# Kernel tuning notes

Hardware: AMD Instinct MI355X
Metric: run time of the kernel (lower is better)

## Reference

```python
import jax, jax.numpy as jnp
import numpy as np

N = 100_000   # nodes
E = 3_200_000 # edges (avg degree 32)
F_NODE = 64
F_EDGE = 16
HID = 64
NEG_SLOPE = 0.2


def _gat_conv(x, src, dst, edge_attr, W, a_src, a_dst, We, a_e, bias, n):
    """PyG GATConv (heads=1, edge_dim, add_self_loops=True fill='mean', eval mode)."""
    # --- add self loops; loop edge_attr = mean of incoming edge_attr per node ---
    deg = jax.ops.segment_sum(jnp.ones((src.shape[0],), x.dtype), dst, num_segments=n)
    loop_attr = jax.ops.segment_sum(edge_attr, dst, num_segments=n)
    loop_attr = jnp.where(deg[:, None] > 0, loop_attr / jnp.maximum(deg, 1.0)[:, None], 0.0)
    loop = jnp.arange(n, dtype=src.dtype)
    src2 = jnp.concatenate([src, loop])
    dst2 = jnp.concatenate([dst, loop])
    ea = jnp.concatenate([edge_attr, loop_attr], axis=0)

    # --- node / edge projections and per-node attention terms ---
    h = x @ W                                   # [N, HID]
    alpha_src = h @ a_src                       # [N]
    alpha_dst = h @ a_dst                       # [N]
    e = ea @ We                                 # [E+N, HID]
    alpha_e = e @ a_e                           # [E+N]

    # --- per-edge logits + segment softmax over destination neighborhoods ---
    logits = jax.nn.leaky_relu(alpha_src[src2] + alpha_dst[dst2] + alpha_e, NEG_SLOPE)
    seg_max = jax.ops.segment_max(logits, dst2, num_segments=n)  # every node has self loop
    ex = jnp.exp(logits - seg_max[dst2])
    denom = jax.ops.segment_sum(ex, dst2, num_segments=n)
    w = ex / denom[dst2]                        # [E+N]

    # --- weighted scatter-aggregate of messages ---
    out = jax.ops.segment_sum(h[src2] * w[:, None], dst2, num_segments=n)
    return out + bias


def setup_inputs() -> dict:
    key = jax.random.key(0)
    ks = jax.random.split(key, 16)
    s = 0.1  # keep logits tame
    return {
        "x": jax.random.normal(ks[0], (N, F_NODE), jnp.float32),
        "edge_index": jax.random.randint(ks[1], (2, E), 0, N, jnp.int32),
        "edge_attr": jax.random.normal(ks[2], (E, F_EDGE), jnp.float32),
        "W1": jax.random.normal(ks[3], (F_NODE, HID), jnp.float32) * s,
        "att_src1": jax.random.normal(ks[4], (HID,), jnp.float32) * s,
        "att_dst1": jax.random.normal(ks[5], (HID,), jnp.float32) * s,
        "We1": jax.random.normal(ks[6], (F_EDGE, HID), jnp.float32) * s,
        "att_edge1": jax.random.normal(ks[7], (HID,), jnp.float32) * s,
        "b1": jnp.zeros((HID,), jnp.float32),
        "W2": jax.random.normal(ks[8], (HID, HID), jnp.float32) * s,
        "att_src2": jax.random.normal(ks[9], (HID,), jnp.float32) * s,
        "att_dst2": jax.random.normal(ks[10], (HID,), jnp.float32) * s,
        "We2": jax.random.normal(ks[11], (F_EDGE, HID), jnp.float32) * s,
        "att_edge2": jax.random.normal(ks[12], (HID,), jnp.float32) * s,
        "b2": jnp.zeros((HID,), jnp.float32),
        "fc_w": jax.random.normal(ks[13], (HID, 1), jnp.float32) * s,
        "fc_b": jnp.zeros((1,), jnp.float32),
    }


def reference(x, edge_index, edge_attr, W1, att_src1, att_dst1, We1, att_edge1, b1,
              W2, att_src2, att_dst2, We2, att_edge2, b2, fc_w, fc_b):
    src, dst = edge_index[0], edge_index[1]
    n = x.shape[0]
    h = jax.nn.elu(_gat_conv(x, src, dst, edge_attr, W1, att_src1, att_dst1, We1, att_edge1, b1, n))
    h = jax.nn.elu(_gat_conv(h, src, dst, edge_attr, W2, att_src2, att_dst2, We2, att_edge2, b2, n))
    return h @ fc_w + fc_b  # [N, 1] logits
```

## Files before the change

kernel.cpp:

```cpp
#include <hip/hip_runtime.h>
#include <hip/hip_bf16.h>
#include <hip/hip_fp16.h>
#include <math.h>
#include <stdint.h>

constexpr int HIDDIM = 64;
constexpr int FEDGE  = 16;
constexpr int BN     = 512;
constexpr int CAP    = 17000;
constexpr int TILE   = 4096;
constexpr int NTA    = 512;
constexpr int EPT    = TILE / NTA;

__global__ void compute_c_kernel(const float* __restrict__ We1, const float* __restrict__ ae1,
                                 const float* __restrict__ We2, const float* __restrict__ ae2,
                                 float* __restrict__ c) {
  int t = threadIdx.x;
  if (t < FEDGE) {
    float s = 0.f;
    for (int j = 0; j < HIDDIM; ++j) s += We1[t * HIDDIM + j] * ae1[j];
    c[t] = s;
  } else if (t < 2 * FEDGE) {
    int k = t - FEDGE;
    float s = 0.f;
    for (int j = 0; j < HIDDIM; ++j) s += We2[k * HIDDIM + j] * ae2[j];
    c[FEDGE + k] = s;
  }
}

__device__ __forceinline__ int pack_ae(float a1, float a2) {
  unsigned lo = __half_as_ushort(__float2half_rn(a1));
  unsigned hi = __half_as_ushort(__float2half_rn(a2));
  return (int)((hi << 16) | lo);
}
template <int SEL>
__device__ __forceinline__ float unpack_ae(int pk) {
  unsigned u = (SEL == 0) ? ((unsigned)pk & 0xFFFFu) : ((unsigned)pk >> 16);
  return __half2float(__ushort_as_half((unsigned short)u));
}

__global__ __launch_bounds__(NTA) void passA_kernel(
    const int* __restrict__ src, const int* __restrict__ dst,
    const float* __restrict__ attr, const float* __restrict__ c,
    int* __restrict__ bucketCursor, int2* __restrict__ P, int E, int nbuck) {
  __shared__ int st_ae[TILE];
  __shared__ int s_key[TILE];
  __shared__ int s_ae[TILE];
  __shared__ unsigned char s_b[TILE];
  __shared__ int cnt[256];
  __shared__ int lbase[512];
  __shared__ int gbase[256];
  __shared__ int wsum[8];
  __shared__ float cs[32];
  int t = threadIdx.x;
  if (t < 32) cs[t] = c[t];
  if (t < nbuck) cnt[t] = 0;
  __syncthreads();
  int e0 = blockIdx.x * TILE;
  int tileCnt = min(TILE, E - e0);

  int d_reg[EPT];
#pragma unroll
  for (int k = 0; k < EPT; ++k) {
    int e = e0 + k * NTA + t;
    d_reg[k] = (e < E) ? dst[e] : -1;
  }
#pragma unroll
  for (int k = 0; k < EPT; ++k) {
    if (d_reg[k] >= 0) atomicAdd(&cnt[d_reg[k] >> 9], 1);
  }
  __syncthreads();

  int lane = t & 63, w = t >> 6;
  int n = (t < nbuck) ? cnt[t] : 0;
  int ret = 0;
  if (n > 0) ret = atomicAdd(&bucketCursor[t], n);
  int incl = n;
#pragma unroll
  for (int d = 1; d < 64; d <<= 1) {
    int tv = __shfl_up(incl, d, 64);
    if (lane >= d) incl += tv;
  }
  if (lane == 63) wsum[w] = incl;
  __syncthreads();
  {
    int woff = 0;
#pragma unroll
    for (int w2 = 0; w2 < 8; ++w2) woff += (w2 < w) ? wsum[w2] : 0;
    lbase[t] = incl - n + woff;
    if (t < nbuck) { gbase[t] = ret; cnt[t] = 0; }
  }

  {
    int q   = t & 3;
    int grp = t >> 2;
    const float4* attr4 = (const float4*)attr;
#pragma unroll
    for (int pass = 0; pass < TILE / 128; ++pass) {
      int el = pass * 128 + grp;
      int e = e0 + el;
      float4 v = make_float4(0.f, 0.f, 0.f, 0.f);
      if (e < E) v = attr4[(size_t)e * 4 + q];
      float a1 = v.x * cs[4*q]    + v.y * cs[4*q+1]    + v.z * cs[4*q+2]    + v.w * cs[4*q+3];
      float a2 = v.x * cs[16+4*q] + v.y * cs[16+4*q+1] + v.z * cs[16+4*q+2] + v.w * cs[16+4*q+3];
      a1 += __shfl_xor(a1, 1, 64); a1 += __shfl_xor(a1, 2, 64);
      a2 += __shfl_xor(a2, 1, 64); a2 += __shfl_xor(a2, 2, 64);
      if (q == 0) st_ae[el] = pack_ae(a1, a2);
    }
  }
  __syncthreads();

#pragma unroll
  for (int k = 0; k < EPT; ++k) {
    int d = d_reg[k];
    if (d < 0) continue;
    int el = k * NTA + t;
    int e = e0 + el;
    int b = d >> 9;
    int sE = src[e];
    int r = atomicAdd(&cnt[b], 1);
    int idx = lbase[b] + r;
    s_key[idx] = sE | ((d & 511) << 20);
    s_ae[idx]  = st_ae[el];
    s_b[idx]   = (unsigned char)b;
  }
  __syncthreads();

  for (int i = t; i < tileCnt; i += NTA) {
    int b = s_b[i];
    int rank = i - lbase[b];
    int pos = gbase[b] + rank;
    if (pos < CAP) P[(size_t)b * CAP + pos] = make_int2(s_key[i], s_ae[i]);
  }
}

__global__ void scan_buckets_kernel(const int* __restrict__ bucketCursor,
                                    int* __restrict__ bucketBase,
                                    int* __restrict__ offsets, int nbuck, int N, int E) {
  __shared__ int s[512];
  int t = threadIdx.x;
  int v = (t < nbuck) ? min(bucketCursor[t], CAP) : 0;
  s[t] = v;
  __syncthreads();
  for (int d = 1; d < 512; d <<= 1) {
    int tv = (t >= d) ? s[t - d] : 0;
    __syncthreads();
    s[t] += tv;
    __syncthreads();
  }
  if (t < nbuck) bucketBase[t] = s[t] - v;
  if (t == 0) offsets[N] = E;
}

__global__ __launch_bounds__(512) void passB_kernel(
    const int2* __restrict__ P, const int* __restrict__ bucketCursor,
    const int* __restrict__ bucketBase, int* __restrict__ offsets,
    int2* __restrict__ EDGS, int N) {
  int b = blockIdx.x;
  int t = threadIdx.x;
  int nodeBase = b * BN;
  int cnt = min(bucketCursor[b], CAP);
  int gbase = bucketBase[b];
  __shared__ int hist[BN];
  __shared__ int cur[BN];
  __shared__ int wsum[8];
  hist[t] = 0;
  __syncthreads();
  const int2* Pb = P + (size_t)b * CAP;
  for (int i = t; i < cnt; i += 512) {
    int dl = (Pb[i].x >> 20) & 511;
    atomicAdd(&hist[dl], 1);
  }
  __syncthreads();
  int deg = hist[t];
  int lane = t & 63, w = t >> 6;
  int incl = deg;
#pragma unroll
  for (int d = 1; d < 64; d <<= 1) {
    int tv = __shfl_up(incl, d, 64);
    if (lane >= d) incl += tv;
  }
  if (lane == 63) wsum[w] = incl;
  __syncthreads();
  int woff = 0;
#pragma unroll
  for (int w2 = 0; w2 < 8; ++w2) woff += (w2 < w) ? wsum[w2] : 0;
  int excl = incl - deg + woff;
  int nodeId = nodeBase + t;
  if (nodeId < N) offsets[nodeId] = gbase + excl;
  cur[t] = gbase + excl;
  __syncthreads();
  for (int i = t; i < cnt; i += 512) {
    int2 r = Pb[i];
    int dl = (r.x >> 20) & 511;
    int pos = atomicAdd(&cur[dl], 1);
    EDGS[pos] = r;
  }
}

template <bool IN16>
__global__ __launch_bounds__(256) void gemm_alpha_kernel(
    const void* __restrict__ Xv, const float* __restrict__ W,
    const float* __restrict__ a_src, const float* __restrict__ a_dst,
    __half2* __restrict__ H, float* __restrict__ alpha_s, float* __restrict__ alpha_d, int n) {
  __shared__ float Ws[HIDDIM * HIDDIM];
  __shared__ float as_s[HIDDIM], ad_s[HIDDIM];
  for (int i = threadIdx.x; i < HIDDIM * HIDDIM; i += blockDim.x) Ws[i] = W[i];
  if (threadIdx.x < HIDDIM) {
    as_s[threadIdx.x] = a_src[threadIdx.x];
    ad_s[threadIdx.x] = a_dst[threadIdx.x];
  }
  __syncthreads();
  int lane = threadIdx.x & 63;
  int wid  = threadIdx.x >> 6;
  int wavesTotal = (blockDim.x >> 6) * gridDim.x;
  for (int row = blockIdx.x * (blockDim.x >> 6) + wid; row < n; row += wavesTotal) {
    float xv;
    if (IN16) xv = __half2float(((const __half*)Xv)[(size_t)row * HIDDIM + lane]);
    else      xv = ((const float*)Xv)[(size_t)row * HIDDIM + lane];
    float acc = 0.f;
#pragma unroll
    for (int k = 0; k < HIDDIM; ++k) {
      float xk = __shfl(xv, k, 64);
      acc = fmaf(xk, Ws[k * HIDDIM + lane], acc);
    }
    float accN = __shfl_xor(acc, 1, 64);
    if (!(lane & 1)) {
      H[(size_t)row * 32 + (lane >> 1)] = __floats2half2_rn(acc, accN);
    }
    float s1 = acc * as_s[lane];
    float s2 = acc * ad_s[lane];
#pragma unroll
    for (int d = 32; d > 0; d >>= 1) {
      s1 += __shfl_xor(s1, d, 64);
      s2 += __shfl_xor(s2, d, 64);
    }
    if (lane == 0) {
      alpha_s[row] = s1;
      alpha_d[row] = s2;
    }
  }
}

__device__ __forceinline__ float leaky(float x) { return (x < 0.f) ? 0.2f * x : x; }
__device__ __forceinline__ float elu(float x) { return (x > 0.f) ? x : (__expf(x) - 1.f); }

template <bool FINAL, int SEL>
__global__ __launch_bounds__(256) void aggregate_kernel(
    const __half2* __restrict__ H, const float* __restrict__ alpha_s, const float* __restrict__ alpha_d,
    const int2* __restrict__ EDGS, const int* __restrict__ offsets,
    const float* __restrict__ bias, const float* __restrict__ fc_w, const float* __restrict__ fc_b,
    void* __restrict__ out, int n) {
  int lane = threadIdx.x & 63;
  int wid  = threadIdx.x >> 6;
  int node = blockIdx.x * (blockDim.x >> 6) + wid;
  if (node >= n) return;
  int off = offsets[node];
  int deg = offsets[node + 1] - off;
  float ad  = alpha_d[node];
  float asn = alpha_s[node];

  if (deg <= 64) {
    int2 ed = make_int2(0, 0);
    if (lane < deg) ed = EDGS[off + lane];
    int   s_l  = ed.x & 0xFFFFF;
    float ae_l = unpack_ae<SEL>(ed.y);
    float as_g = (lane < deg) ? alpha_s[s_l] : 0.f;
    float lg_l = (lane < deg) ? leaky(as_g + ad + ae_l) : -INFINITY;
    float aesum = (lane < deg) ? ae_l : 0.f;
    float lmax = lg_l;
#pragma unroll
    for (int d = 32; d > 0; d >>= 1) {
      lmax = fmaxf(lmax, __shfl_xor(lmax, d, 64));
      aesum += __shfl_xor(aesum, d, 64);
    }
    float self_ae = (deg > 0) ? aesum / (float)deg : 0.f;
    float slg = leaky(asn + ad + self_ae);
    float m = fmaxf(lmax, slg);

    float ex_l = (lane < deg) ? __expf(lg_l - m) : 0.f;
    float dsum = ex_l;
#pragma unroll
    for (int d = 32; d > 0; d >>= 1) dsum += __shfl_xor(dsum, d, 64);
    float exs = __expf(slg - m);
    float denom = dsum + exs;

    int half = lane >> 5;
    int c32  = lane & 31;

    float selfw = (half == 0) ? exs : 0.f;
    float2 hv = __half22float2(H[(size_t)node * 32 + c32]);
    float2 acc2;
    acc2.x = selfw * hv.x;
    acc2.y = selfw * hv.y;

    int jj = 0;
    for (; jj + 16 <= deg; jj += 16) {
      int   si[8]; float ei[8];
#pragma unroll
      for (int k = 0; k < 8; ++k) {
        si[k] = __shfl(s_l, jj + 2 * k + half, 64);
        ei[k] = __shfl(ex_l, jj + 2 * k + half, 64);
      }
      float2 hh[8];
#pragma unroll
      for (int k = 0; k < 8; ++k) hh[k] = __half22float2(H[(size_t)si[k] * 32 + c32]);
#pragma unroll
      for (int k = 0; k < 8; ++k) {
        acc2.x = fmaf(ei[k], hh[k].x, acc2.x);
        acc2.y = fmaf(ei[k], hh[k].y, acc2.y);
      }
    }
    for (; jj + 8 <= deg; jj += 8) {
      int j0 = jj + half, j1 = jj + 2 + half, j2 = jj + 4 + half, j3 = jj + 6 + half;
      int   sa = __shfl(s_l, j0, 64),  sb = __shfl(s_l, j1, 64);
      int   sc = __shfl(s_l, j2, 64),  sd = __shfl(s_l, j3, 64);
      float ea = __shfl(ex_l, j0, 64), eb = __shfl(ex_l, j1, 64);
      float ec = __shfl(ex_l, j2, 64), ef = __shfl(ex_l, j3, 64);
      float2 ha = __half22float2(H[(size_t)sa * 32 + c32]);
      float2 hb = __half22float2(H[(size_t)sb * 32 + c32]);
      float2 hc = __half22float2(H[(size_t)sc * 32 + c32]);
      float2 hd = __half22float2(H[(size_t)sd * 32 + c32]);
      acc2.x = fmaf(ea, ha.x, acc2.x); acc2.y = fmaf(ea, ha.y, acc2.y);
      acc2.x = fmaf(eb, hb.x, acc2.x); acc2.y = fmaf(eb, hb.y, acc2.y);
      acc2.x = fmaf(ec, hc.x, acc2.x); acc2.y = fmaf(ec, hc.y, acc2.y);
      acc2.x = fmaf(ef, hd.x, acc2.x); acc2.y = fmaf(ef, hd.y, acc2.y);
    }
    for (; jj < deg; jj += 2) {
      int j = jj + half;
      int   sj = __shfl(s_l, j, 64);
      float ej = __shfl(ex_l, j, 64);
      float2 hj = __half22float2(H[(size_t)sj * 32 + c32]);
      acc2.x = fmaf(ej, hj.x, acc2.x);
      acc2.y = fmaf(ej, hj.y, acc2.y);
    }
    acc2.x += __shfl_xor(acc2.x, 32, 64);
    acc2.y += __shfl_xor(acc2.y, 32, 64);

    const float2* bi2 = (const float2*)bias;
    float2 bv = bi2[c32];
    float rx = elu(acc2.x / denom + bv.x);
    float ry = elu(acc2.y / denom + bv.y);
    if (!FINAL) {
      if (half == 0) {
        ((__half2*)out)[(size_t)node * 32 + c32] = __floats2half2_rn(rx, ry);
      }
    } else {
      const float2* fw2 = (const float2*)fc_w;
      float2 fv = fw2[c32];
      float s1 = rx * fv.x + ry * fv.y;
#pragma unroll
      for (int d = 16; d > 0; d >>= 1) s1 += __shfl_xor(s1, d, 64);
      if (lane == 0) ((float*)out)[node] = s1 + fc_b[0];
    }
    return;
  }

  {
    const __half* Hh = (const __half*)H;
    float lmax = -INFINITY, aesum = 0.f;
    for (int base = 0; base < deg; base += 64) {
      int i = base + lane;
      if (i < deg) {
        int2 ed = EDGS[off + i];
        int s = ed.x & 0xFFFFF;
        float ae = unpack_ae<SEL>(ed.y);
        float lg = leaky(alpha_s[s] + ad + ae);
        lmax = fmaxf(lmax, lg);
        aesum += ae;
      }
    }
#pragma unroll
    for (int d = 32; d > 0; d >>= 1) {
      lmax = fmaxf(lmax, __shfl_xor(lmax, d, 64));
      aesum += __shfl_xor(aesum, d, 64);
    }
    float self_ae = aesum / (float)deg;
    float slg = leaky(asn + ad + self_ae);
    float m = fmaxf(lmax, slg);
    float exs = __expf(slg - m);
    float dsum = 0.f;
    float acc = exs * __half2float(Hh[(size_t)node * HIDDIM + lane]);
    for (int base = 0; base < deg; base += 64) {
      int i = base + lane;
      int cnt = min(64, deg - base);
      int2 ed = make_int2(0, 0);
      if (i < deg) ed = EDGS[off + i];
      int   s_l  = ed.x & 0xFFFFF;
      float ae_l = unpack_ae<SEL>(ed.y);
      float ex_l = (lane < cnt) ? __expf(leaky(alpha_s[s_l] + ad + ae_l) - m) : 0.f;
      dsum += ex_l;
      for (int j = 0; j < cnt; ++j) {
        int   sj = __shfl(s_l, j, 64);
        float ej = __shfl(ex_l, j, 64);
        acc = fmaf(ej, __half2float(Hh[(size_t)sj * HIDDIM + lane]), acc);
      }
    }
#pragma unroll
    for (int d = 32; d > 0; d >>= 1) dsum += __shfl_xor(dsum, d, 64);
    float denom = dsum + exs;

    float res = elu(acc / denom + bias[lane]);
    if (!FINAL) {
      ((__half*)out)[(size_t)node * HIDDIM + lane] = __float2half_rn(res);
    } else {
      float s1 = res * fc_w[lane];
#pragma unroll
      for (int d = 32; d > 0; d >>= 1) s1 += __shfl_xor(s1, d, 64);
      if (lane == 0) ((float*)out)[node] = s1 + fc_b[0];
    }
  }
}

extern "C" void kernel_launch(void* const* d_in, const int* in_sizes, int n_in,
                              void* d_out, int out_size, void* d_ws, size_t ws_size,
                              hipStream_t stream) {
  const float* x    = (const float*)d_in[0];
  const int*   ei   = (const int*)d_in[1];
  const float* attr = (const float*)d_in[2];
  const float* W1   = (const float*)d_in[3];
  const float* as1  = (const float*)d_in[4];
  const float* ad1  = (const float*)d_in[5];
  const float* We1  = (const float*)d_in[6];
  const float* ae1  = (const float*)d_in[7];
  const float* b1   = (const float*)d_in[8];
  const float* W2   = (const float*)d_in[9];
  const float* as2  = (const float*)d_in[10];
  const float* ad2  = (const float*)d_in[11];
  const float* We2  = (const float*)d_in[12];
  const float* ae2  = (const float*)d_in[13];
  const float* b2   = (const float*)d_in[14];
  const float* fcw  = (const float*)d_in[15];
  const float* fcb  = (const float*)d_in[16];

  const int N = in_sizes[0] / HIDDIM;
  const int E = in_sizes[1] / 2;
  const int NBUCK = (N + BN - 1) / BN;

  char* p = (char*)d_ws;
  auto alloc = [&](size_t bytes) -> void* {
    void* r = (void*)p;
    p += (bytes + 255) & ~(size_t)255;
    return r;
  };
  float*  c            = (float*)alloc(32 * sizeof(float));
  int*    bucketCursor = (int*)alloc(512 * 4);
  int*    bucketBase   = (int*)alloc(((size_t)NBUCK + 1) * 4);
  int*    offsets      = (int*)alloc(((size_t)N + 1) * 4);
  float*  alpha_s      = (float*)alloc((size_t)N * 4);
  float*  alpha_d      = (float*)alloc((size_t)N * 4);
  int2*   EDGS         = (int2*)alloc((size_t)E * 8);
  size_t  regionBytes  = (size_t)NBUCK * CAP * 8;
  size_t  hBytes       = ((size_t)N * HIDDIM * 2 + 255) & ~(size_t)255;
  size_t  x2Bytes      = (size_t)N * HIDDIM * 2;
  if (hBytes + x2Bytes > regionBytes) regionBytes = hBytes + x2Bytes;
  char*   region       = (char*)alloc(regionBytes);
  int2*   P            = (int2*)region;
  __half2* H           = (__half2*)region;
  __half2* X2          = (__half2*)(region + hBytes);

  const int* srcp = ei;
  const int* dstp = ei + E;

  hipMemsetAsync(bucketCursor, 0, 512 * 4, stream);

  compute_c_kernel<<<1, 64, 0, stream>>>(We1, ae1, We2, ae2, c);

  int ablocks = (E + TILE - 1) / TILE;
  passA_kernel<<<ablocks, NTA, 0, stream>>>(srcp, dstp, attr, c, bucketCursor, P, E, NBUCK);
  scan_buckets_kernel<<<1, 512, 0, stream>>>(bucketCursor, bucketBase, offsets, NBUCK, N, E);
  passB_kernel<<<NBUCK, 512, 0, stream>>>(P, bucketCursor, bucketBase, offsets, EDGS, N);

  int aggBlocks = (N + 3) / 4;

  gemm_alpha_kernel<false><<<2048, 256, 0, stream>>>(x, W1, as1, ad1, H, alpha_s, alpha_d, N);
  aggregate_kernel<false, 0><<<aggBlocks, 256, 0, stream>>>(H, alpha_s, alpha_d, EDGS,
                                                            offsets, b1, nullptr, nullptr, X2, N);
  gemm_alpha_kernel<true><<<2048, 256, 0, stream>>>(X2, W2, as2, ad2, H, alpha_s, alpha_d, N);
  aggregate_kernel<true, 1><<<aggBlocks, 256, 0, stream>>>(H, alpha_s, alpha_d, EDGS,
                                                           offsets, b2, fcw, fcb, d_out, N);
}
```

Measured before the change: 448.6 us.

## Fuse layer-1 node GEMM into edge bucketing kernel as extra blocks

Merges the first layer's node projection and attention-term computation into the edge bucketing pass by appending extra blocks that run the GEMM while the other blocks bucket edges. This requires un-aliasing the bucket staging buffer from the H and X2 buffers, which adds workspace memory. The bucket-cursor memset is folded into the small coefficient kernel. The intent is to cut a launch and let the bandwidth-bound GEMM overlap with the scatter-heavy edge pass.

After: 431.9 us. 1.04x faster.

```diff
diff --git a/kernel.cpp b/kernel.cpp
--- a/kernel.cpp
+++ b/kernel.cpp
@@ -11,11 +11,13 @@
 constexpr int TILE   = 4096;
 constexpr int NTA    = 512;
 constexpr int EPT    = TILE / NTA;
+constexpr int GBLK   = 1536;
 
 __global__ void compute_c_kernel(const float* __restrict__ We1, const float* __restrict__ ae1,
                                  const float* __restrict__ We2, const float* __restrict__ ae2,
-                                 float* __restrict__ c) {
+                                 float* __restrict__ c, int* __restrict__ bucketCursor) {
   int t = threadIdx.x;
+  if (t < 512) bucketCursor[t] = 0;
   if (t < FEDGE) {
     float s = 0.f;
     for (int j = 0; j < HIDDIM; ++j) s += We1[t * HIDDIM + j] * ae1[j];
@@ -39,98 +41,144 @@
   return __half2float(__ushort_as_half((unsigned short)u));
 }
 
-__global__ __launch_bounds__(NTA) void passA_kernel(
+__global__ __launch_bounds__(NTA) void passA_gemm_kernel(
     const int* __restrict__ src, const int* __restrict__ dst,
     const float* __restrict__ attr, const float* __restrict__ c,
-    int* __restrict__ bucketCursor, int2* __restrict__ P, int E, int nbuck) {
-  __shared__ int st_ae[TILE];
-  __shared__ int s_key[TILE];
-  __shared__ int s_ae[TILE];
-  __shared__ unsigned char s_b[TILE];
-  __shared__ int cnt[256];
-  __shared__ int lbase[512];
-  __shared__ int gbase[256];
-  __shared__ int wsum[8];
-  __shared__ float cs[32];
+    int* __restrict__ bucketCursor, int2* __restrict__ P, int E, int nbuck, int ablocks,
+    const float* __restrict__ X, const float* __restrict__ W,
+    const float* __restrict__ a_src, const float* __restrict__ a_dst,
+    __half2* __restrict__ H, float* __restrict__ alpha_s, float* __restrict__ alpha_d, int N) {
+  __shared__ char smem[57856];
   int t = threadIdx.x;
-  if (t < 32) cs[t] = c[t];
-  if (t < nbuck) cnt[t] = 0;
-  __syncthreads();
-  int e0 = blockIdx.x * TILE;
-  int tileCnt = min(TILE, E - e0);
-
-  int d_reg[EPT];
-#pragma unroll
-  for (int k = 0; k < EPT; ++k) {
-    int e = e0 + k * NTA + t;
-    d_reg[k] = (e < E) ? dst[e] : -1;
-  }
-#pragma unroll
-  for (int k = 0; k < EPT; ++k) {
-    if (d_reg[k] >= 0) atomicAdd(&cnt[d_reg[k] >> 9], 1);
-  }
-  __syncthreads();
-
-  int lane = t & 63, w = t >> 6;
-  int n = (t < nbuck) ? cnt[t] : 0;
-  int ret = 0;
-  if (n > 0) ret = atomicAdd(&bucketCursor[t], n);
-  int incl = n;
-#pragma unroll
-  for (int d = 1; d < 64; d <<= 1) {
-    int tv = __shfl_up(incl, d, 64);
-    if (lane >= d) incl += tv;
-  }
-  if (lane == 63) wsum[w] = incl;
-  __syncthreads();
-  {
-    int woff = 0;
-#pragma unroll
-    for (int w2 = 0; w2 < 8; ++w2) woff += (w2 < w) ? wsum[w2] : 0;
-    lbase[t] = incl - n + woff;
-    if (t < nbuck) { gbase[t] = ret; cnt[t] = 0; }
-  }
-
-  {
-    int q   = t & 3;
-    int grp = t >> 2;
-    const float4* attr4 = (const float4*)attr;
-#pragma unroll
-    for (int pass = 0; pass < TILE / 128; ++pass) {
-      int el = pass * 128 + grp;
+
+  if (blockIdx.x < ablocks) {
+    int*  st_ae = (int*)smem;
+    int*  s_key = st_ae + TILE;
+    int*  s_ae  = s_key + TILE;
+    unsigned char* s_b = (unsigned char*)(s_ae + TILE);
+    int*  cnt   = (int*)(s_b + TILE);
+    int*  lbase = cnt + 256;
+    int*  gbase = lbase + 512;
+    int*  wsum  = gbase + 256;
+    float* cs   = (float*)(wsum + 8);
+
+    if (t < 32) cs[t] = c[t];
+    if (t < nbuck) cnt[t] = 0;
+    __syncthreads();
+    int e0 = blockIdx.x * TILE;
+    int tileCnt = min(TILE, E - e0);
+
+    int d_reg[EPT];
+#pragma unroll
+    for (int k = 0; k < EPT; ++k) {
+      int e = e0 + k * NTA + t;
+      d_reg[k] = (e < E) ? dst[e] : -1;
+    }
+#pragma unroll
+    for (int k = 0; k < EPT; ++k) {
+      if (d_reg[k] >= 0) atomicAdd(&cnt[d_reg[k] >> 9], 1);
+    }
+    __syncthreads();
+
+    int lane = t & 63, w = t >> 6;
+    int n = (t < nbuck) ? cnt[t] : 0;
+    int ret = 0;
+    if (n > 0) ret = atomicAdd(&bucketCursor[t], n);
+    int incl = n;
+#pragma unroll
+    for (int d = 1; d < 64; d <<= 1) {
+      int tv = __shfl_up(incl, d, 64);
+      if (lane >= d) incl += tv;
+    }
+    if (lane == 63) wsum[w] = incl;
+    __syncthreads();
+    {
+      int woff = 0;
+#pragma unroll
+      for (int w2 = 0; w2 < 8; ++w2) woff += (w2 < w) ? wsum[w2] : 0;
+      lbase[t] = incl - n + woff;
+      if (t < nbuck) { gbase[t] = ret; cnt[t] = 0; }
+    }
+
+    {
+      int q   = t & 3;
+      int grp = t >> 2;
+      const float4* attr4 = (const float4*)attr;
+#pragma unroll
+      for (int pass = 0; pass < TILE / 128; ++pass) {
+        int el = pass * 128 + grp;
+        int e = e0 + el;
+        float4 v = make_float4(0.f, 0.f, 0.f, 0.f);
+        if (e < E) v = attr4[(size_t)e * 4 + q];
+        float a1 = v.x * cs[4*q]    + v.y * cs[4*q+1]    + v.z * cs[4*q+2]    + v.w * cs[4*q+3];
+        float a2 = v.x * cs[16+4*q] + v.y * cs[16+4*q+1] + v.z * cs[16+4*q+2] + v.w * cs[16+4*q+3];
+        a1 += __shfl_xor(a1, 1, 64); a1 += __shfl_xor(a1, 2, 64);
+        a2 += __shfl_xor(a2, 1, 64); a2 += __shfl_xor(a2, 2, 64);
+        if (q == 0) st_ae[el] = pack_ae(a1, a2);
+      }
+    }
+    __syncthreads();
+
+#pragma unroll
+    for (int k = 0; k < EPT; ++k) {
+      int d = d_reg[k];
+      if (d < 0) continue;
+      int el = k * NTA + t;
       int e = e0 + el;
-      float4 v = make_float4(0.f, 0.f, 0.f, 0.f);
-      if (e < E) v = attr4[(size_t)e * 4 + q];
-      float a1 = v.x * cs[4*q]    + v.y * cs[4*q+1]    + v.z * cs[4*q+2]    + v.w * cs[4*q+3];
-      float a2 = v.x * cs[16+4*q] + v.y * cs[16+4*q+1] + v.z * cs[16+4*q+2] + v.w * cs[16+4*q+3];
-      a1 += __shfl_xor(a1, 1, 64); a1 += __shfl_xor(a1, 2, 64);
-      a2 += __shfl_xor(a2, 1, 64); a2 += __shfl_xor(a2, 2, 64);
-      if (q == 0) st_ae[el] = pack_ae(a1, a2);
-    }
-  }
-  __syncthreads();
-
-#pragma unroll
-  for (int k = 0; k < EPT; ++k) {
-    int d = d_reg[k];
-    if (d < 0) continue;
-    int el = k * NTA + t;
-    int e = e0 + el;
-    int b = d >> 9;
-    int sE = src[e];
-    int r = atomicAdd(&cnt[b], 1);
-    int idx = lbase[b] + r;
-    s_key[idx] = sE | ((d & 511) << 20);
-    s_ae[idx]  = st_ae[el];
-    s_b[idx]   = (unsigned char)b;
-  }
-  __syncthreads();
-
-  for (int i = t; i < tileCnt; i += NTA) {
-    int b = s_b[i];
-    int rank = i - lbase[b];
-    int pos = gbase[b] + rank;
-    if (pos < CAP) P[(size_t)b * CAP + pos] = make_int2(s_key[i], s_ae[i]);
+      int b = d >> 9;
+      int sE = src[e];
+      int r = atomicAdd(&cnt[b], 1);
+      int idx = lbase[b] + r;
+      s_key[idx] = sE | ((d & 511) << 20);
+      s_ae[idx]  = st_ae[el];
+      s_b[idx]   = (unsigned char)b;
+    }
+    __syncthreads();
+
+    for (int i = t; i < tileCnt; i += NTA) {
+      int b = s_b[i];
+      int rank = i - lbase[b];
+      int pos = gbase[b] + rank;
+      if (pos < CAP) P[(size_t)b * CAP + pos] = make_int2(s_key[i], s_ae[i]);
+    }
+  } else {
+    float* Ws   = (float*)smem;
+    float* as_s = Ws + HIDDIM * HIDDIM;
+    float* ad_s = as_s + HIDDIM;
+    for (int i = t; i < HIDDIM * HIDDIM; i += NTA) Ws[i] = W[i];
+    if (t < HIDDIM) {
+      as_s[t] = a_src[t];
+      ad_s[t] = a_dst[t];
+    }
+    __syncthreads();
+    int lane = t & 63;
+    int wid  = t >> 6;
+    int gbid = blockIdx.x - ablocks;
+    int wavesTotal = 8 * GBLK;
+    for (int row = gbid * 8 + wid; row < N; row += wavesTotal) {
+      float xv = X[(size_t)row * HIDDIM + lane];
+      float acc = 0.f;
+#pragma unroll
+      for (int k = 0; k < HIDDIM; ++k) {
+        float xk = __shfl(xv, k, 64);
+        acc = fmaf(xk, Ws[k * HIDDIM + lane], acc);
+      }
+      float accN = __shfl_xor(acc, 1, 64);
+      if (!(lane & 1)) {
+        H[(size_t)row * 32 + (lane >> 1)] = __floats2half2_rn(acc, accN);
+      }
+      float s1 = acc * as_s[lane];
+      float s2 = acc * ad_s[lane];
+#pragma unroll
+      for (int d = 32; d > 0; d >>= 1) {
+        s1 += __shfl_xor(s1, d, 64);
+        s2 += __shfl_xor(s2, d, 64);
+      }
+      if (lane == 0) {
+        alpha_s[row] = s1;
+        alpha_d[row] = s2;
+      }
+    }
   }
 }
 
@@ -450,30 +498,25 @@
   float*  alpha_s      = (float*)alloc((size_t)N * 4);
   float*  alpha_d      = (float*)alloc((size_t)N * 4);
   int2*   EDGS         = (int2*)alloc((size_t)E * 8);
-  size_t  regionBytes  = (size_t)NBUCK * CAP * 8;
-  size_t  hBytes       = ((size_t)N * HIDDIM * 2 + 255) & ~(size_t)255;
-  size_t  x2Bytes      = (size_t)N * HIDDIM * 2;
-  if (hBytes + x2Bytes > regionBytes) regionBytes = hBytes + x2Bytes;
-  char*   region       = (char*)alloc(regionBytes);
-  int2*   P            = (int2*)region;
-  __half2* H           = (__half2*)region;
-  __half2* X2          = (__half2*)(region + hBytes);
+  int2*   P            = (int2*)alloc((size_t)NBUCK * CAP * 8);
+  __half2* H           = (__half2*)alloc((size_t)N * 32 * 4);
+  __half2* X2          = (__half2*)alloc((size_t)N * 32 * 4);
 
   const int* srcp = ei;
   const int* dstp = ei + E;
 
-  hipMemsetAsync(bucketCursor, 0, 512 * 4, stream);
-
-  compute_c_kernel<<<1, 64, 0, stream>>>(We1, ae1, We2, ae2, c);
+  compute_c_kernel<<<1, 512, 0, stream>>>(We1, ae1, We2, ae2, c, bucketCursor);
 
   int ablocks = (E + TILE - 1) / TILE;
-  passA_kernel<<<ablocks, NTA, 0, stream>>>(srcp, dstp, attr, c, bucketCursor, P, E, NBUCK);
+  passA_gemm_kernel<<<ablocks + GBLK, NTA, 0, stream>>>(
+      srcp, dstp, attr, c, bucketCursor, P, E, NBUCK, ablocks,
+      x, W1, as1, ad1, H, alpha_s, alpha_d, N);
+
   scan_buckets_kernel<<<1, 512, 0, stream>>>(bucketCursor, bucketBase, offsets, NBUCK, N, E);
   passB_kernel<<<NBUCK, 512, 0, stream>>>(P, bucketCursor, bucketBase, offsets, EDGS, N);
 
   int aggBlocks = (N + 3) / 4;
 
-  gemm_alpha_kernel<false><<<2048, 256, 0, stream>>>(x, W1, as1, ad1, H, alpha_s, alpha_d, N);
   aggregate_kernel<false, 0><<<aggBlocks, 256, 0, stream>>>(H, alpha_s, alpha_d, EDGS,
                                                             offsets, b1, nullptr, nullptr, X2, N);
   gemm_alpha_kernel<true><<<2048, 256, 0, stream>>>(X2, W2, as2, ad2, H, alpha_s, alpha_d, N);
```
